# Kernel tuning notes

Measured on AMD Instinct MI355X. Metric: run time of the kernel, lower is better.

The kernel has to match this reference:

```python
import jax, jax.numpy as jnp
import numpy as np

SAMPLE_RATE = 24000.0
HARMONIC_NUM = 8
SINE_AMP = 0.1
DIM = HARMONIC_NUM + 1
BATCH, LENGTH = 16, 480000


def setup_inputs() -> dict:
    key = jax.random.key(0)
    k1, k2, k3 = jax.random.split(key, 3)
    u = jax.random.uniform(k1, (BATCH, LENGTH), dtype=jnp.float32)
    voiced = (jax.random.uniform(k2, (BATCH, LENGTH)) > 0.2).astype(jnp.float32)
    f0 = (80.0 + 400.0 * u) * voiced
    rand_ini = jax.random.uniform(k3, (BATCH, 1, DIM), dtype=jnp.float32)
    return {"f0": f0, "rand_ini": rand_ini}


def reference(f0, rand_ini):
    # f0: [B, L] -> [B, L, 1]
    f0 = f0[..., None]
    harmonics = jnp.arange(1, DIM + 1, dtype=f0.dtype).reshape(1, 1, -1)  # [1,1,DIM]
    rad_values = jnp.mod(f0 * harmonics / SAMPLE_RATE, 1.0)              # [B,L,DIM]
    rad_values = rad_values.at[:, 0:1, :].add(rand_ini)                  # random initial phase
    phase = jnp.cumsum(rad_values, axis=1) * (2.0 * jnp.pi)              # [B,L,DIM]
    uv = (f0 > 0).astype(f0.dtype)                                       # [B,L,1]
    sine_waves = jnp.sin(phase) * SINE_AMP * uv                          # fused scale+mask
    return sine_waves, uv
```

## Files before the change

kernel.cpp:

```cpp
#include <hip/hip_runtime.h>
#include <math.h>

#define BATCH 16
#define LEN 480000
#define NDIM 9
#define CHUNK 1024
#define NCHUNK 469
#define AMP 0.1f

typedef float vfloat4 __attribute__((ext_vector_type(4)));

__device__ __forceinline__ float hw_fract(float x) {
#if __has_builtin(__builtin_amdgcn_fractf)
  return __builtin_amdgcn_fractf(x);
#else
  return x - floorf(x);
#endif
}
__device__ __forceinline__ float hw_sin1(float x) {
#if __has_builtin(__builtin_amdgcn_sinf)
  return __builtin_amdgcn_sinf(x);
#else
  return __sinf(x * 6.283185307179586f);
#endif
}

__global__ __launch_bounds__(256) void sg_partial(const float* __restrict__ f0,
                                                  double* __restrict__ part) {
  const int c = blockIdx.x, b = blockIdx.y, t = threadIdx.x;
  const int i4 = c * 256 + t;
  float4 v = make_float4(0.f, 0.f, 0.f, 0.f);
  if (i4 < LEN / 4) v = ((const float4*)(f0 + (size_t)b * LEN))[i4];
  double s = (double)((v.x + v.y) + (v.z + v.w));
#pragma unroll
  for (int d = 32; d > 0; d >>= 1) s += __shfl_down(s, d, 64);
  __shared__ double ws[4];
  if ((t & 63) == 0) ws[t >> 6] = s;
  __syncthreads();
  if (t == 0) part[(size_t)b * NCHUNK + c] = (ws[0] + ws[1]) + (ws[2] + ws[3]);
}

__global__ __launch_bounds__(256) void sg_main(const float* __restrict__ f0,
                                               const float* __restrict__ rand_ini,
                                               const double* __restrict__ part,
                                               float* __restrict__ out) {
  const int c = blockIdx.x, b = blockIdx.y, t = threadIdx.x;
  const int lane = t & 63, w = t >> 6;

  __shared__ __align__(16) float Pl[CHUNK + 4];
  __shared__ __align__(16) float Al[CHUNK + 4];
  __shared__ float2 Hl[NDIM];
  __shared__ float wsc[4];
  __shared__ double dred[4];

  const int i4 = c * 256 + t;
  float4 v = make_float4(0.f, 0.f, 0.f, 0.f);
  if (i4 < LEN / 4) v = ((const float4*)(f0 + (size_t)b * LEN))[i4];
  const float gs = (v.x + v.y) + (v.z + v.w);

  const double* prow = part + (size_t)b * NCHUNK;
  double s = 0.0;
  if (t < c) s += prow[t];
  if (t + 256 < c) s += prow[t + 256];
#pragma unroll
  for (int d = 32; d > 0; d >>= 1) s += __shfl_down(s, d, 64);
  if (lane == 0) dred[w] = s;

  float x = gs;
#pragma unroll
  for (int d = 1; d < 64; d <<= 1) {
    float y = __shfl_up(x, d, 64);
    if (lane >= d) x += y;
  }
  if (lane == 63) wsc[w] = x;
  __syncthreads();

  if (t < NDIM) {
    const double cb = (dred[0] + dred[1]) + (dred[2] + dred[3]);
    const double hs = (double)(t + 1) * (1.0 / 24000.0);
    double p0 = (double)rand_ini[b * NDIM + t] + hs * cb;
    p0 -= floor(p0);
    Hl[t] = make_float2((float)p0, (float)hs);
  }

  const float t0 = wsc[0], t1 = wsc[1], t2 = wsc[2];
  const float wpre = (w > 0 ? t0 : 0.f) + (w > 1 ? t1 : 0.f) + (w > 2 ? t2 : 0.f);
  const float Pex = wpre + (x - gs);

  const float p0v = Pex + v.x;
  const float p1v = p0v + v.y;
  const float p2v = p1v + v.z;
  const float p3v = p2v + v.w;
  {
    vfloat4 pq; pq.x = p0v; pq.y = p1v; pq.z = p2v; pq.w = p3v;
    *(vfloat4*)&Pl[4 * t] = pq;
    vfloat4 aq;
    aq.x = (v.x > 0.f) ? AMP : 0.f;
    aq.y = (v.y > 0.f) ? AMP : 0.f;
    aq.z = (v.z > 0.f) ? AMP : 0.f;
    aq.w = (v.w > 0.f) ? AMP : 0.f;
    *(vfloat4*)&Al[4 * t] = aq;
  }
  __syncthreads();

  vfloat4* out4 = (vfloat4*)out;
  const int base = c * CHUNK;
  const int valid = min(CHUNK, LEN - base);
  const int nf4 = (valid * NDIM) >> 2;
  const size_t gb4 = ((size_t)b * LEN * NDIM + (size_t)base * NDIM) >> 2;

  const int f0i = 4 * t;
  const int q0 = f0i / 9;
  const int r0 = f0i % 9;

#pragma unroll
  for (int k = 0; k < 9; ++k) {
    const int idx = k * 256 + t;
    const int K9 = (1024 * k) / 9;
    const int rk = (1024 * k) % 9;
    const int rsum = r0 + rk;
    const int carry = (rsum >= 9) ? 1 : 0;
    const int e = q0 + K9 + carry;
    const int r = rsum - 9 * carry;
    const float PA = Pl[e], PB = Pl[e + 1];
    const float aA = Al[e], aB = Al[e + 1];
    float res[4];
#pragma unroll
    for (int j = 0; j < 4; ++j) {
      const int h = r + j;
      const bool crs = (h >= 9);
      const int hh = crs ? h - 9 : h;
      const float2 ph = Hl[hh];
      const float Pe = crs ? PB : PA;
      const float am = crs ? aB : aA;
      res[j] = am * hw_sin1(hw_fract(ph.x + ph.y * Pe));
    }
    if (idx < nf4) {
      vfloat4 q; q.x = res[0]; q.y = res[1]; q.z = res[2]; q.w = res[3];
      __builtin_nontemporal_store(q, &out4[gb4 + idx]);
    }
  }

  const size_t uv4_base = ((size_t)BATCH * LEN * NDIM) / 4 + ((size_t)b * LEN) / 4;
  if (i4 < LEN / 4) {
    vfloat4 u;
    u.x = (v.x > 0.f) ? 1.f : 0.f;
    u.y = (v.y > 0.f) ? 1.f : 0.f;
    u.z = (v.z > 0.f) ? 1.f : 0.f;
    u.w = (v.w > 0.f) ? 1.f : 0.f;
    __builtin_nontemporal_store(u, &out4[uv4_base + i4]);
  }
}

extern "C" void kernel_launch(void* const* d_in, const int* in_sizes, int n_in,
                              void* d_out, int out_size, void* d_ws, size_t ws_size,
                              hipStream_t stream) {
  const float* f0 = (const float*)d_in[0];
  const float* rand_ini = (const float*)d_in[1];
  float* out = (float*)d_out;

  double* part = (double*)d_ws;

  dim3 grid(NCHUNK, BATCH);
  sg_partial<<<grid, 256, 0, stream>>>(f0, part);
  sg_main<<<grid, 256, 0, stream>>>(f0, rand_ini, part, out);
}
```

Before: 323.1 us.

## Fuse partial-sum and main kernels into one persistent cooperative kernel with grid sync

Replaces the two-kernel launch (chunk partial sums, then phase/sine generation) with one cooperative persistent kernel of 1024 blocks. Each block loops over up to 8 chunks, first writing chunk sums, then doing a grid-wide sync, then running the main phase and sine loop. The loop uses double-buffered shared memory and a lighter LDS barrier. The goal is to remove the second launch and the inter-kernel gap. The cost is a grid sync, fewer resident blocks working in a persistent loop, and a fallback to the old path if the cooperative launch fails.

```diff
diff --git a/kernel.cpp b/kernel.cpp
--- a/kernel.cpp
+++ b/kernel.cpp
@@ -1,4 +1,5 @@
 #include <hip/hip_runtime.h>
+#include <hip/hip_cooperative_groups.h>
 #include <math.h>
 
 #define BATCH 16
@@ -6,7 +7,12 @@
 #define NDIM 9
 #define CHUNK 1024
 #define NCHUNK 469
+#define TOTCH (NCHUNK * BATCH)
+#define NBLK 1024
+#define MAXJ 8
 #define AMP 0.1f
+
+namespace cg = cooperative_groups;
 
 typedef float vfloat4 __attribute__((ext_vector_type(4)));
 
@@ -23,6 +29,13 @@
 #else
   return __sinf(x * 6.283185307179586f);
 #endif
+}
+
+__device__ __forceinline__ void bar_lds() {
+  asm volatile("s_waitcnt lgkmcnt(0)" ::: "memory");
+  __builtin_amdgcn_s_barrier();
+  __builtin_amdgcn_sched_barrier(0);
+  asm volatile("" ::: "memory");
 }
 
 __global__ __launch_bounds__(256) void sg_partial(const float* __restrict__ f0,
@@ -108,7 +121,6 @@
   const int valid = min(CHUNK, LEN - base);
   const int nf4 = (valid * NDIM) >> 2;
   const size_t gb4 = ((size_t)b * LEN * NDIM + (size_t)base * NDIM) >> 2;
-
   const int f0i = 4 * t;
   const int q0 = f0i / 9;
   const int r0 = f0i % 9;
@@ -152,16 +164,158 @@
   }
 }
 
+__global__ __launch_bounds__(256, 4) void sg_fused(const float* __restrict__ f0,
+                                                   const float* __restrict__ rand_ini,
+                                                   double* __restrict__ part,
+                                                   float* __restrict__ out) {
+  const int k = blockIdx.x, t = threadIdx.x;
+  const int lane = t & 63, w = t >> 6;
+
+  __shared__ double ws1[4];
+  __shared__ __align__(16) float Pl[2][CHUNK + 4];
+  __shared__ __align__(16) float Al[2][CHUNK + 4];
+  __shared__ float2 Hl[2][NDIM];
+  __shared__ float wsc[2][4];
+  __shared__ double dred[2][4];
+
+  for (int j = 0; j < MAXJ; ++j) {
+    const int m = k + j * NBLK;
+    if (m >= TOTCH) break;
+    const int b = m / NCHUNK, c = m - b * NCHUNK;
+    const int i4 = c * 256 + t;
+    float4 v = make_float4(0.f, 0.f, 0.f, 0.f);
+    if (i4 < LEN / 4) v = ((const float4*)(f0 + (size_t)b * LEN))[i4];
+    double s = (double)((v.x + v.y) + (v.z + v.w));
+#pragma unroll
+    for (int d = 32; d > 0; d >>= 1) s += __shfl_down(s, d, 64);
+    if (lane == 0) ws1[w] = s;
+    __syncthreads();
+    if (t == 0) part[m] = (ws1[0] + ws1[1]) + (ws1[2] + ws1[3]);
+    __syncthreads();
+  }
+
+  cg::this_grid().sync();
+
+  vfloat4* out4 = (vfloat4*)out;
+  const size_t uvall = ((size_t)BATCH * LEN * NDIM) / 4;
+
+  for (int j = 0; j < MAXJ; ++j) {
+    const int m = k + j * NBLK;
+    if (m >= TOTCH) break;
+    const int p = j & 1;
+    const int b = m / NCHUNK, c = m - b * NCHUNK;
+    const int i4 = c * 256 + t;
+
+    float4 v = make_float4(0.f, 0.f, 0.f, 0.f);
+    if (i4 < LEN / 4) v = ((const float4*)(f0 + (size_t)b * LEN))[i4];
+    const float gs = (v.x + v.y) + (v.z + v.w);
+
+    const double* prow = part + (size_t)b * NCHUNK;
+    double s = 0.0;
+    if (t < c) s += prow[t];
+    if (t + 256 < c) s += prow[t + 256];
+#pragma unroll
+    for (int d = 32; d > 0; d >>= 1) s += __shfl_down(s, d, 64);
+    if (lane == 0) dred[p][w] = s;
+
+    float x = gs;
+#pragma unroll
+    for (int d = 1; d < 64; d <<= 1) {
+      float y = __shfl_up(x, d, 64);
+      if (lane >= d) x += y;
+    }
+    if (lane == 63) wsc[p][w] = x;
+    bar_lds();
+
+    if (t < NDIM) {
+      const double cb = (dred[p][0] + dred[p][1]) + (dred[p][2] + dred[p][3]);
+      const double hs = (double)(t + 1) * (1.0 / 24000.0);
+      double p0 = (double)rand_ini[b * NDIM + t] + hs * cb;
+      p0 -= floor(p0);
+      Hl[p][t] = make_float2((float)p0, (float)hs);
+    }
+
+    const float t0 = wsc[p][0], t1 = wsc[p][1], t2 = wsc[p][2];
+    const float wpre = (w > 0 ? t0 : 0.f) + (w > 1 ? t1 : 0.f) + (w > 2 ? t2 : 0.f);
+    const float Pex = wpre + (x - gs);
+
+    const float p0v = Pex + v.x;
+    const float p1v = p0v + v.y;
+    const float p2v = p1v + v.z;
+    const float p3v = p2v + v.w;
+    {
+      vfloat4 pq; pq.x = p0v; pq.y = p1v; pq.z = p2v; pq.w = p3v;
+      *(vfloat4*)&Pl[p][4 * t] = pq;
+      vfloat4 aq;
+      aq.x = (v.x > 0.f) ? AMP : 0.f;
+      aq.y = (v.y > 0.f) ? AMP : 0.f;
+      aq.z = (v.z > 0.f) ? AMP : 0.f;
+      aq.w = (v.w > 0.f) ? AMP : 0.f;
+      *(vfloat4*)&Al[p][4 * t] = aq;
+    }
+    bar_lds();
+
+    const int base = c * CHUNK;
+    const int valid = min(CHUNK, LEN - base);
+    const int nf4 = (valid * NDIM) >> 2;
+    const size_t gb4 = ((size_t)b * LEN * NDIM + (size_t)base * NDIM) >> 2;
+    const int f0i = 4 * t;
+    const int q0 = f0i / 9;
+    const int r0 = f0i % 9;
+
+#pragma unroll
+    for (int kk = 0; kk < 9; ++kk) {
+      const int idx = kk * 256 + t;
+      const int K9 = (1024 * kk) / 9;
+      const int rk = (1024 * kk) % 9;
+      const int rsum = r0 + rk;
+      const int carry = (rsum >= 9) ? 1 : 0;
+      const int e = q0 + K9 + carry;
+      const int r = rsum - 9 * carry;
+      const float PA = Pl[p][e], PB = Pl[p][e + 1];
+      const float aA = Al[p][e], aB = Al[p][e + 1];
+      float res[4];
+#pragma unroll
+      for (int jj = 0; jj < 4; ++jj) {
+        const int h = r + jj;
+        const bool crs = (h >= 9);
+        const int hh = crs ? h - 9 : h;
+        const float2 ph = Hl[p][hh];
+        const float Pe = crs ? PB : PA;
+        const float am = crs ? aB : aA;
+        res[jj] = am * hw_sin1(hw_fract(ph.x + ph.y * Pe));
+      }
+      if (idx < nf4) {
+        vfloat4 q; q.x = res[0]; q.y = res[1]; q.z = res[2]; q.w = res[3];
+        __builtin_nontemporal_store(q, &out4[gb4 + idx]);
+      }
+    }
+
+    if (i4 < LEN / 4) {
+      vfloat4 u;
+      u.x = (v.x > 0.f) ? 1.f : 0.f;
+      u.y = (v.y > 0.f) ? 1.f : 0.f;
+      u.z = (v.z > 0.f) ? 1.f : 0.f;
+      u.w = (v.w > 0.f) ? 1.f : 0.f;
+      __builtin_nontemporal_store(u, &out4[uvall + ((size_t)b * LEN) / 4 + i4]);
+    }
+  }
+}
+
 extern "C" void kernel_launch(void* const* d_in, const int* in_sizes, int n_in,
                               void* d_out, int out_size, void* d_ws, size_t ws_size,
                               hipStream_t stream) {
   const float* f0 = (const float*)d_in[0];
   const float* rand_ini = (const float*)d_in[1];
   float* out = (float*)d_out;
-
   double* part = (double*)d_ws;
 
-  dim3 grid(NCHUNK, BATCH);
-  sg_partial<<<grid, 256, 0, stream>>>(f0, part);
-  sg_main<<<grid, 256, 0, stream>>>(f0, rand_ini, part, out);
-}
+  void* args[] = {(void*)&f0, (void*)&rand_ini, (void*)&part, (void*)&out};
+  hipError_t e = hipLaunchCooperativeKernel((const void*)sg_fused, dim3(NBLK),
+                                            dim3(256), args, 0, stream);
+  if (e != hipSuccess) {
+    dim3 grid(NCHUNK, BATCH);
+    sg_partial<<<grid, 256, 0, stream>>>(f0, part);
+    sg_main<<<grid, 256, 0, stream>>>(f0, rand_ini, part, out);
+  }
+}
```

Measured after the change: 455.8 us. 41.1% more time.
